# Kernel tuning notes

Hardware: AMD Instinct MI355X
Metric: run time of the kernel (lower is better)

## Reference

```python
import jax, jax.numpy as jnp
import numpy as np

B, N, IN_DIM, HID, HEADS, K = 2, 2048, 1024, 512, 8, 8
HD = HID // HEADS
EPS = 1e-5
SCALE = float(1.0 / np.sqrt(HD))

def _ln(x, g, b):
    m = jnp.mean(x, -1, keepdims=True)
    v = jnp.var(x, -1, keepdims=True)
    return (x - m) * jax.lax.rsqrt(v + EPS) * g + b

def setup_inputs() -> dict:
    key = jax.random.key(0)
    ks = jax.random.split(key, 40)
    def p(k, shape):
        return jax.random.normal(k, shape, jnp.float32) * 0.02
    z = lambda *s: jnp.zeros(s, jnp.float32)
    o = lambda *s: jnp.ones(s, jnp.float32)
    return {
        "x": jax.random.normal(ks[0], (B, N, IN_DIM), jnp.float32),
        # fc_start: Linear(in,hid) + GLU Linear(hid,2*hid)
        "w_start": p(ks[1], (HID, IN_DIM)), "b_start": z(HID),
        "glu_w": p(ks[2], (2 * HID, HID)), "glu_b": z(2 * HID),
        # 2 GCN layers (stacked on leading axis)
        "gcn_w": p(ks[3], (2, HID, HID)), "gcn_b": z(2, HID),
        "gcn_g": o(2, HID), "gcn_beta": z(2, HID),
        # 2 transformer layers
        "qkv_w": p(ks[4], (2, 3 * HID, HID)), "qkv_b": z(2, 3 * HID),
        "out_w": p(ks[5], (2, HID, HID)), "out_b": z(2, HID),
        "ln1_g": o(2, HID), "ln1_b": z(2, HID),
        "ffn_w1": p(ks[6], (2, 2 * HID, HID)), "ffn_b1": z(2, 2 * HID),
        "ffn_w2": p(ks[7], (2, HID, 2 * HID)), "ffn_b2": z(2, HID),
        "ln2_g": o(2, HID), "ln2_b": z(2, HID),
        # fusion, attention pooling, classifier
        "fus_w": p(ks[8], (HID, 2 * HID)), "fus_b": z(HID),
        "attn_w1": p(ks[9], (256, HID)), "attn_b1": z(256),
        "attn_w2": p(ks[10], (1, 256)), "attn_b2": z(1),
        "cls_w1": p(ks[11], (HID // 2, HID)), "cls_b1": z(HID // 2),
        "cls_w2": p(ks[12], (1, HID // 2)), "cls_b2": z(1),
    }

def reference(x, w_start, b_start, glu_w, glu_b, gcn_w, gcn_b, gcn_g, gcn_beta,
              qkv_w, qkv_b, out_w, out_b, ln1_g, ln1_b, ffn_w1, ffn_b1,
              ffn_w2, ffn_b2, ln2_g, ln2_b, fus_w, fus_b,
              attn_w1, attn_b1, attn_w2, attn_b2,
              cls_w1, cls_b1, cls_w2, cls_b2):
    # fc_start: Linear -> GLU (dropout off in eval)
    h = x @ w_start.T + b_start
    vg = h @ glu_w.T + glu_b
    val, gate = jnp.split(vg, 2, -1)
    h = val * jax.nn.sigmoid(gate)                      # [B,N,HID]

    # dynamic KNN graph: cdist + topk + scatter + sym-normalize
    sq = jnp.sum(h * h, -1)
    d2 = sq[:, :, None] + sq[:, None, :] - 2.0 * jnp.einsum('bnc,bmc->bnm', h, h)
    dist = jnp.sqrt(jnp.maximum(d2, 0.0))
    _, idx = jax.lax.top_k(-dist, K + 1)                # nearest K+1 (incl self)
    bi = jnp.arange(B)[:, None, None]
    ri = jnp.arange(N)[None, :, None]
    adj = jnp.zeros((B, N, N), h.dtype).at[bi, ri, idx].set(1.0)
    rs = jnp.sum(adj, -1)
    dinv = jnp.where(rs > 0, rs ** -0.5, 0.0)
    adj = adj * dinv[:, :, None] * dinv[:, None, :]     # == D^-1/2 A D^-1/2

    # GCN branch
    hg = h
    for i in range(2):
        s = hg @ gcn_w[i].T + gcn_b[i]
        o = jnp.einsum('bnm,bmc->bnc', adj, s)
        o = _ln(o, gcn_g[i], gcn_beta[i])
        hg = jax.nn.leaky_relu(o, 0.2) + hg

    # Transformer branch (post-LN)
    ht = h
    for i in range(2):
        qkv = ht @ qkv_w[i].T + qkv_b[i]
        q, k_, v = jnp.split(qkv, 3, -1)
        q = q.reshape(B, N, HEADS, HD)
        k_ = k_.reshape(B, N, HEADS, HD)
        v = v.reshape(B, N, HEADS, HD)
        att = jax.nn.softmax(jnp.einsum('bqhd,bkhd->bhqk', q, k_) * SCALE, -1)
        ao = jnp.einsum('bhqk,bkhd->bqhd', att, v).reshape(B, N, HID)
        ao = ao @ out_w[i].T + out_b[i]
        ht = _ln(ht + ao, ln1_g[i], ln1_b[i])
        ff = jax.nn.gelu(ht @ ffn_w1[i].T + ffn_b1[i], approximate=False) @ ffn_w2[i].T + ffn_b2[i]
        ht = _ln(ht + ff, ln2_g[i], ln2_b[i])

    hf = jnp.concatenate([hg, ht], -1) @ fus_w.T + fus_b  # [B,N,HID]

    # gated attention pooling
    a = jnp.tanh(hf @ attn_w1.T + attn_b1) @ attn_w2.T + attn_b2
    a = jax.nn.softmax(a, axis=1)                       # [B,N,1]
    M = jnp.sum(hf * a, axis=1)                         # [B,HID]

    logits = jax.nn.elu(M @ cls_w1.T + cls_b1) @ cls_w2.T + cls_b2  # [B,1]
    return logits, a, M
```

## Files before the change

kernel.cpp:

```cpp
#include <hip/hip_runtime.h>
#include <hip/hip_bf16.h>
#include <math.h>

#define NSEQ 2048
#define ROWS 4096
#define KNN 9
#define MB (1ull << 20)

typedef short bh8 __attribute__((ext_vector_type(8)));
typedef float f4v __attribute__((ext_vector_type(4)));
typedef unsigned long long u64k;

__device__ __forceinline__ short f2bf(float f) {
    union { float f; unsigned u; } v; v.f = f;
    unsigned r = (v.u + 0x7fffu + ((v.u >> 16) & 1u)) >> 16;
    return (short)r;
}
__device__ __forceinline__ float b2f(short s) {
    union { unsigned u; float f; } v; v.u = ((unsigned)(unsigned short)s) << 16; return v.f;
}

__device__ __forceinline__ void gload16(const void* g, void* l) {
    __builtin_amdgcn_global_load_lds(
        (const __attribute__((address_space(1))) void*)g,
        (__attribute__((address_space(3))) void*)l, 16, 0, 0);
}

__device__ __forceinline__ float blockReduceSum(float v, float* red) {
    int tid = threadIdx.x;
    red[tid] = v; __syncthreads();
    for (int s = 128; s > 0; s >>= 1) {
        if (tid < s) red[tid] += red[tid + s];
        __syncthreads();
    }
    float r = red[0]; __syncthreads();
    return r;
}

struct CvtArgs { const float* src[10]; short* dst[10]; int n4[10]; };
__global__ __launch_bounds__(256) void cvt_k(CvtArgs a) {
    int s = blockIdx.y;
    const float* sp = a.src[s]; short* dp = a.dst[s]; int n = a.n4[s];
    for (int i = blockIdx.x * 256 + threadIdx.x; i < n; i += gridDim.x * 256) {
        float4 v = ((const float4*)sp)[i];
        short4 o; o.x = f2bf(v.x); o.y = f2bf(v.y); o.z = f2bf(v.z); o.w = f2bf(v.w);
        ((short4*)dp)[i] = o;
    }
}

template <int OUTMODE>
__global__ __launch_bounds__(256) void mfma_gemm(
        const short* __restrict__ A, const short* __restrict__ W,
        const float* __restrict__ bias, float* __restrict__ Cf, short* __restrict__ Cb,
        int M, int N, int K)
{
    __shared__ short As[2][64 * 64];
    __shared__ short Bs[2][64 * 64];
    int tid = threadIdx.x;
    int wv = tid >> 6, l = tid & 63;
    int g = l >> 4, c = l & 15;
    int wr = wv >> 1, wc = wv & 1;
    int bm = blockIdx.y * 64, bn = blockIdx.x * 64;
    int sr = l >> 3, sc = ((l & 7) ^ sr) * 8;
    const short* Ap = A + (size_t)(bm + wv * 16 + sr) * K + sc;
    const short* Wp = W + (size_t)(bn + wv * 16 + sr) * K + sc;
    int ldsB = (wv * 16) * 64;

    #define GSTAGE(buf, k0) { \
        gload16(Ap + (k0), &As[buf][ldsB]); \
        gload16(Ap + (size_t)8 * K + (k0), &As[buf][ldsB + 8 * 64]); \
        gload16(Wp + (k0), &Bs[buf][ldsB]); \
        gload16(Wp + (size_t)8 * K + (k0), &Bs[buf][ldsB + 8 * 64]); }

    f4v acc[2][2] = {};
    GSTAGE(0, 0);
    __syncthreads();
    int nk = K >> 6;
    for (int t = 0; t < nk; ++t) {
        int cur = t & 1;
        if (t + 1 < nk) GSTAGE(cur ^ 1, (t + 1) << 6);
        #pragma unroll
        for (int ks = 0; ks < 2; ++ks) {
            bh8 af[2], bf_[2];
            #pragma unroll
            for (int mi = 0; mi < 2; ++mi) {
                int row = wr * 32 + mi * 16 + c;
                af[mi] = *(const bh8*)(&As[cur][row * 64 + (((ks * 4 + g) ^ (c & 7)) * 8)]);
            }
            #pragma unroll
            for (int ni = 0; ni < 2; ++ni) {
                int row = wc * 32 + ni * 16 + c;
                bf_[ni] = *(const bh8*)(&Bs[cur][row * 64 + (((ks * 4 + g) ^ (c & 7)) * 8)]);
            }
            #pragma unroll
            for (int mi = 0; mi < 2; ++mi)
                #pragma unroll
                for (int ni = 0; ni < 2; ++ni)
                    acc[mi][ni] = __builtin_amdgcn_mfma_f32_16x16x32_bf16(af[mi], bf_[ni], acc[mi][ni], 0, 0, 0);
        }
        __syncthreads();
    }
    #undef GSTAGE
    short* Kb_  = (OUTMODE == 3) ? Cb + 2097152 : nullptr;
    short* Vt_  = (OUTMODE == 3) ? Cb + 4194304 : nullptr;
    #pragma unroll
    for (int mi = 0; mi < 2; ++mi) {
        int row = bm + wr * 32 + mi * 16 + g * 4;
        #pragma unroll
        for (int ni = 0; ni < 2; ++ni) {
            int col = bn + wc * 32 + ni * 16 + c;
            float bv = bias[col];
            #pragma unroll
            for (int rr = 0; rr < 4; ++rr) {
                float v = acc[mi][ni][rr] + bv;
                if (OUTMODE == 0) Cf[(size_t)(row + rr) * N + col] = v;
                else if (OUTMODE == 1) Cb[(size_t)(row + rr) * N + col] = f2bf(v);
                else if (OUTMODE == 2) {
                    Cf[(size_t)(row + rr) * N + col] = v;
                    Cb[(size_t)(row + rr) * N + col] = f2bf(v);
                } else if (OUTMODE == 3) {
                    int b = (row + rr) >> 11, n = (row + rr) & 2047;
                    if (col < 512) {
                        int h = col >> 6, d = col & 63;
                        Cb[(((size_t)(b * 8 + h) * NSEQ + n) << 6) + d] = f2bf(v * 0.18033688f);
                    } else if (col < 1024) {
                        int cc = col - 512, h = cc >> 6, d = cc & 63;
                        Kb_[(((size_t)(b * 8 + h) * NSEQ + n) << 6) + d] = f2bf(v);
                    } else {
                        int cc = col - 1024, h = cc >> 6, d = cc & 63;
                        Vt_[(((size_t)(b * 8 + h) * NSEQ + n) << 6) + d] = f2bf(v);
                    }
                } else if (OUTMODE == 4) {
                    Cb[(size_t)(row + rr) * N + col] = f2bf(0.5f * v * (1.f + erff(v * 0.70710678118654752f)));
                } else if (OUTMODE == 5) {
                    Cf[(size_t)(row + rr) * N + col] = tanhf(v);
                }
            }
        }
    }
}

__global__ __launch_bounds__(256) void mfma_gram(
        const short* __restrict__ Hi, const short* __restrict__ Lo,
        const float* __restrict__ SQ, float* __restrict__ D2)
{
    __shared__ short HiR[64 * 64], LoR[64 * 64], HiC[64 * 64], LoC[64 * 64];
    int tid = threadIdx.x;
    int wv = tid >> 6, l = tid & 63;
    int g = l >> 4, c = l & 15;
    int wr = wv >> 1, wc = wv & 1;
    int bm = blockIdx.y * 64, bn = blockIdx.x * 64;
    int sr = l >> 3, sc = ((l & 7) ^ sr) * 8;
    const short* hiR = Hi + (size_t)(bm + wv * 16 + sr) * 512 + sc;
    const short* loR = Lo + (size_t)(bm + wv * 16 + sr) * 512 + sc;
    const short* hiC = Hi + (size_t)(bn + wv * 16 + sr) * 512 + sc;
    const short* loC = Lo + (size_t)(bn + wv * 16 + sr) * 512 + sc;
    int ldsOff = (wv * 16) * 64;
    f4v acc[2][2] = {};
    for (int k0 = 0; k0 < 512; k0 += 64) {
        __syncthreads();
        gload16(hiR + k0, HiR + ldsOff);
        gload16(hiR + (size_t)8 * 512 + k0, HiR + ldsOff + 8 * 64);
        gload16(loR + k0, LoR + ldsOff);
        gload16(loR + (size_t)8 * 512 + k0, LoR + ldsOff + 8 * 64);
        gload16(hiC + k0, HiC + ldsOff);
        gload16(hiC + (size_t)8 * 512 + k0, HiC + ldsOff + 8 * 64);
        gload16(loC + k0, LoC + ldsOff);
        gload16(loC + (size_t)8 * 512 + k0, LoC + ldsOff + 8 * 64);
        __syncthreads();
        #pragma unroll
        for (int ks = 0; ks < 2; ++ks) {
            bh8 hr[2], lr_[2], hc[2], lc[2];
            #pragma unroll
            for (int mi = 0; mi < 2; ++mi) {
                int o = (wr * 32 + mi * 16 + c) * 64 + (((ks * 4 + g) ^ (c & 7)) * 8);
                hr[mi] = *(const bh8*)(HiR + o);
                lr_[mi] = *(const bh8*)(LoR + o);
            }
            #pragma unroll
            for (int ni = 0; ni < 2; ++ni) {
                int o = (wc * 32 + ni * 16 + c) * 64 + (((ks * 4 + g) ^ (c & 7)) * 8);
                hc[ni] = *(const bh8*)(HiC + o);
                lc[ni] = *(const bh8*)(LoC + o);
            }
            #pragma unroll
            for (int mi = 0; mi < 2; ++mi)
                #pragma unroll
                for (int ni = 0; ni < 2; ++ni) {
                    acc[mi][ni] = __builtin_amdgcn_mfma_f32_16x16x32_bf16(hr[mi], hc[ni], acc[mi][ni], 0, 0, 0);
                    acc[mi][ni] = __builtin_amdgcn_mfma_f32_16x16x32_bf16(hr[mi], lc[ni], acc[mi][ni], 0, 0, 0);
                    acc[mi][ni] = __builtin_amdgcn_mfma_f32_16x16x32_bf16(lr_[mi], hc[ni], acc[mi][ni], 0, 0, 0);
                }
        }
    }
    #pragma unroll
    for (int mi = 0; mi < 2; ++mi) {
        int row = bm + wr * 32 + mi * 16 + g * 4;
        #pragma unroll
        for (int ni = 0; ni < 2; ++ni) {
            int col = bn + wc * 32 + ni * 16 + c;
            float sqc = SQ[col];
            #pragma unroll
            for (int rr = 0; rr < 4; ++rr)
                D2[(size_t)(row + rr) * NSEQ + col] = SQ[row + rr] + sqc - 2.f * acc[mi][ni][rr];
        }
    }
}

__global__ __launch_bounds__(256) void topk9_k(const float* __restrict__ D2, int* __restrict__ idx)
{
    int n = blockIdx.x, tid = threadIdx.x;
    __shared__ u64k lists[256][9];
    u64k a[8];
    union { float f; unsigned u; } cv;
    #pragma unroll
    for (int j = 0; j < 8; ++j) {
        int mcol = tid + j * 256;
        cv.f = fmaxf(D2[(size_t)n * NSEQ + mcol], 0.f);
        a[j] = ((u64k)cv.u << 32) | (unsigned)mcol;
    }
    #define CE(i,j) { u64k x = a[i], y = a[j]; bool t = x < y; a[i] = t ? x : y; a[j] = t ? y : x; }
    CE(0,1) CE(2,3) CE(4,5) CE(6,7)
    CE(0,2) CE(1,3) CE(4,6) CE(5,7)
    CE(1,2) CE(5,6)
    CE(0,4) CE(1,5) CE(2,6) CE(3,7)
    CE(2,4) CE(3,5)
    CE(1,2) CE(3,4) CE(5,6)
    #undef CE
    #pragma unroll
    for (int j = 0; j < 8; ++j) lists[tid][j] = a[j];
    lists[tid][8] = ~0ull;
    __syncthreads();
    for (int s = 128; s >= 1; s >>= 1) {
        if (tid < s) {
            u64k out[9];
            u64k* Al = lists[tid];
            u64k* Bl = lists[tid + s];
            int ia = 0, ib = 0;
            #pragma unroll
            for (int o = 0; o < 9; ++o) {
                u64k av = Al[ia], bv = Bl[ib];
                bool t = av <= bv;
                out[o] = t ? av : bv;
                ia += t; ib += !t;
            }
            #pragma unroll
            for (int o = 0; o < 9; ++o) Al[o] = out[o];
        }
        __syncthreads();
    }
    if (tid < 9) idx[n * KNN + tid] = (int)(lists[0][tid] & 0xffffffffu);
}

__global__ __launch_bounds__(256) void gcn_post(
        const float* __restrict__ s, const int* __restrict__ idx,
        const float* __restrict__ g, const float* __restrict__ be,
        float* __restrict__ hg, short* __restrict__ hgb)
{
    int row = blockIdx.x, tid = threadIdx.x;
    int bb = row >> 11;
    __shared__ float os[512];
    __shared__ float red[256];
    int id[KNN];
    #pragma unroll
    for (int j = 0; j < KNN; ++j) id[j] = idx[row * KNN + j] + (bb << 11);
    for (int c = tid; c < 512; c += 256) {
        float acc = 0.f;
        #pragma unroll
        for (int j = 0; j < KNN; ++j) acc += s[((size_t)id[j] << 9) + c];
        os[c] = acc * (1.f / 9.f);
    }
    __syncthreads();
    float mean = blockReduceSum(os[tid] + os[tid + 256], red) * (1.f / 512.f);
    float d0 = os[tid] - mean, d1 = os[tid + 256] - mean;
    float var = blockReduceSum(d0 * d0 + d1 * d1, red) * (1.f / 512.f);
    float rs = rsqrtf(var + 1e-5f);
    size_t base = (size_t)row << 9;
    for (int c = tid; c < 512; c += 256) {
        float y = (os[c] - mean) * rs * g[c] + be[c];
        y = y > 0.f ? y : 0.2f * y;
        float nv = y + hg[base + c];
        hg[base + c] = nv;
        hgb[base + c] = f2bf(nv);
    }
}

__global__ __launch_bounds__(256) void ln_res(
        float* __restrict__ x, const float* __restrict__ r,
        const float* __restrict__ g, const float* __restrict__ b, short* __restrict__ xb)
{
    int row = blockIdx.x, tid = threadIdx.x;
    __shared__ float xs[512];
    __shared__ float red[256];
    size_t base = (size_t)row << 9;
    for (int c = tid; c < 512; c += 256) xs[c] = x[base + c] + r[base + c];
    __syncthreads();
    float mean = blockReduceSum(xs[tid] + xs[tid + 256], red) * (1.f / 512.f);
    float d0 = xs[tid] - mean, d1 = xs[tid + 256] - mean;
    float var = blockReduceSum(d0 * d0 + d1 * d1, red) * (1.f / 512.f);
    float rs = rsqrtf(var + 1e-5f);
    for (int c = tid; c < 512; c += 256) {
        float y = (xs[c] - mean) * rs * g[c] + b[c];
        x[base + c] = y;
        xb[base + c] = f2bf(y);
    }
}

__global__ __launch_bounds__(256) void vtr_k(const short* __restrict__ Vtmp, short* __restrict__ Vt)
{
    int nt = blockIdx.x, bh = blockIdx.y;
    int t = threadIdx.x;
    #pragma unroll
    for (int it = 0; it < 2; ++it) {
        int idx = it * 256 + t;
        int d = idx >> 3, nc = (idx & 7) * 8;
        short tmp[8];
        #pragma unroll
        for (int j = 0; j < 8; ++j)
            tmp[j] = Vtmp[(((size_t)bh * NSEQ + nt * 64 + nc + j) << 6) + d];
        *(bh8*)(Vt + (((size_t)bh * 64 + d) << 11) + nt * 64 + nc) = *(const bh8*)tmp;
    }
}

__global__ __launch_bounds__(256) void flash_attn(
        const short* __restrict__ Qb, const short* __restrict__ Kb,
        const short* __restrict__ Vt, float* __restrict__ Op, float* __restrict__ Ml)
{
    __shared__ short Ks[2][4096];
    __shared__ short Vs[2][4096];
    __shared__ char Pl[4][2048];
    int tid = threadIdx.x;
    int wid = tid >> 6, lane = tid & 63;
    int g = lane >> 4, c = lane & 15;
    int s = blockIdx.y, bh = blockIdx.z;
    int q0 = blockIdx.x * 64 + wid * 16;
    char* myP = Pl[wid];
    int srow = lane >> 3;
    int sc8 = ((lane & 7) ^ srow) * 8;
    int w8 = wid * 8;

    const short* KbB = Kb + ((size_t)bh * NSEQ + s * (NSEQ / 2)) * 64;
    const short* VtB = Vt + (size_t)bh * 64 * NSEQ + s * (NSEQ / 2);

    const short* qbase = Qb + ((size_t)bh * NSEQ + q0 + c) * 64 + g * 8;
    bh8 qa0 = *(const bh8*)(qbase);
    bh8 qa1 = *(const bh8*)(qbase + 32);

    bh8 ones;
    #pragma unroll
    for (int j = 0; j < 8; ++j) ones[j] = (short)0x3F80;

    f4v o0 = {0,0,0,0}, o1 = {0,0,0,0}, o2 = {0,0,0,0}, o3 = {0,0,0,0};
    f4v ol = {0,0,0,0};
    float m[4] = {-INFINITY,-INFINITY,-INFINITY,-INFINITY};

    #define FSTAGE(buf, kt) { \
        const short* kp_ = KbB + (size_t)(kt) * 64 * 64; \
        gload16(kp_ + (size_t)(w8 + srow) * 64 + sc8,        &Ks[buf][w8 * 64]); \
        gload16(kp_ + (size_t)(32 + w8 + srow) * 64 + sc8,   &Ks[buf][(32 + w8) * 64]); \
        const short* vp_ = VtB + (size_t)(kt) * 64; \
        gload16(vp_ + (size_t)(w8 + srow) * NSEQ + sc8,      &Vs[buf][w8 * 64]); \
        gload16(vp_ + (size_t)(32 + w8 + srow) * NSEQ + sc8, &Vs[buf][(32 + w8) * 64]); }

    FSTAGE(0, 0);
    __syncthreads();
    for (int t = 0; t < 16; ++t) {
        int cur = t & 1;
        if (t < 15) FSTAGE(cur ^ 1, t + 1);
        f4v sv[4];
        #pragma unroll
        for (int cb = 0; cb < 4; ++cb) {
            int row = cb * 16 + c;
            const short* kr = &Ks[cur][row * 64];
            bh8 kb0 = *(const bh8*)(kr + ((g ^ (row & 7)) * 8));
            bh8 kb1 = *(const bh8*)(kr + (((4 + g) ^ (row & 7)) * 8));
            f4v a = {0,0,0,0};
            a = __builtin_amdgcn_mfma_f32_16x16x32_bf16(qa0, kb0, a, 0, 0, 0);
            a = __builtin_amdgcn_mfma_f32_16x16x32_bf16(qa1, kb1, a, 0, 0, 0);
            sv[cb] = a;
        }
        float mt[4];
        #pragma unroll
        for (int r = 0; r < 4; ++r) {
            float v = fmaxf(fmaxf(sv[0][r], sv[1][r]), fmaxf(sv[2][r], sv[3][r]));
            v = fmaxf(v, __shfl_xor(v, 1));
            v = fmaxf(v, __shfl_xor(v, 2));
            v = fmaxf(v, __shfl_xor(v, 4));
            v = fmaxf(v, __shfl_xor(v, 8));
            mt[r] = v;
        }
        bool need = (mt[0] > m[0] + 6.f) | (mt[1] > m[1] + 6.f) |
                    (mt[2] > m[2] + 6.f) | (mt[3] > m[3] + 6.f);
        if (__any(need)) {
            f4v alv;
            #pragma unroll
            for (int r = 0; r < 4; ++r) {
                float mn = fmaxf(m[r], mt[r]);
                alv[r] = __builtin_amdgcn_exp2f(m[r] - mn);
                m[r] = mn;
            }
            o0 *= alv; o1 *= alv; o2 *= alv; o3 *= alv; ol *= alv;
        }
        #pragma unroll
        for (int cb = 0; cb < 4; ++cb) {
            #pragma unroll
            for (int r = 0; r < 4; ++r) {
                float p = __builtin_amdgcn_exp2f(sv[cb][r] - m[r]);
                unsigned pk;
                asm("v_cvt_pk_bf16_f32 %0, %1, %2" : "=v"(pk) : "v"(p), "v"(p));
                int row = g * 4 + r;
                int byte = row * 128 + (((cb * 16 + c) * 2) ^ ((row & 7) << 4));
                *(short*)(myP + byte) = (short)pk;
            }
        }
        bh8 pa0 = *(const bh8*)(myP + c * 128 + (( 0 + g * 16) ^ ((c & 7) << 4)));
        bh8 pa1 = *(const bh8*)(myP + c * 128 + ((64 + g * 16) ^ ((c & 7) << 4)));
        ol = __builtin_amdgcn_mfma_f32_16x16x32_bf16(pa0, ones, ol, 0, 0, 0);
        ol = __builtin_amdgcn_mfma_f32_16x16x32_bf16(pa1, ones, ol, 0, 0, 0);
        #pragma unroll
        for (int db = 0; db < 4; ++db) {
            int row = db * 16 + c;
            const short* vr = &Vs[cur][row * 64];
            bh8 vb0 = *(const bh8*)(vr + ((g ^ (row & 7)) * 8));
            bh8 vb1 = *(const bh8*)(vr + (((4 + g) ^ (row & 7)) * 8));
            f4v* op = (db == 0) ? &o0 : (db == 1) ? &o1 : (db == 2) ? &o2 : &o3;
            *op = __builtin_amdgcn_mfma_f32_16x16x32_bf16(pa0, vb0, *op, 0, 0, 0);
            *op = __builtin_amdgcn_mfma_f32_16x16x32_bf16(pa1, vb1, *op, 0, 0, 0);
        }
        __syncthreads();
    }
    #undef FSTAGE
    #pragma unroll
    for (int r = 0; r < 4; ++r) {
        size_t rb = (((size_t)(s * 16 + bh) * NSEQ) + q0 + g * 4 + r) * 64 + c;
        Op[rb]      = o0[r];
        Op[rb + 16] = o1[r];
        Op[rb + 32] = o2[r];
        Op[rb + 48] = o3[r];
    }
    if (c == 0) {
        #pragma unroll
        for (int r = 0; r < 4; ++r) {
            size_t mb = (((size_t)(s * 16 + bh) * NSEQ) + q0 + g * 4 + r) * 2;
            Ml[mb] = m[r]; Ml[mb + 1] = ol[r];
        }
    }
}

__global__ __launch_bounds__(256) void merge_k(const float* __restrict__ Op, const float* __restrict__ Ml,
                                               short* __restrict__ aob)
{
    int idx = blockIdx.x * 256 + threadIdx.x;
    int d = idx & 63, q = (idx >> 6) & 2047, bh = idx >> 17;
    size_t r0 = (size_t)bh * NSEQ + q;
    size_t r1 = (size_t)(16 + bh) * NSEQ + q;
    float m0 = Ml[r0 * 2], l0 = Ml[r0 * 2 + 1];
    float m1 = Ml[r1 * 2], l1 = Ml[r1 * 2 + 1];
    float M = fmaxf(m0, m1);
    float w0 = __builtin_amdgcn_exp2f(m0 - M), w1 = __builtin_amdgcn_exp2f(m1 - M);
    float L = l0 * w0 + l1 * w1;
    float v = (Op[r0 * 64 + d] * w0 + Op[r1 * 64 + d] * w1) / L;
    int b = bh >> 3, h = bh & 7;
    aob[((size_t)(b * NSEQ + q)) * 512 + h * 64 + d] = f2bf(v);
}

__global__ __launch_bounds__(256) void glu_row_k(const float* __restrict__ vg, float* __restrict__ h,
        float* __restrict__ hgf, short* __restrict__ hi, short* __restrict__ lo,
        float* __restrict__ sq) {
    int row = blockIdx.x, tid = threadIdx.x;
    __shared__ float red[256];
    size_t vb = (size_t)row << 10;
    size_t hb = (size_t)row << 9;
    float ss = 0.f;
    #pragma unroll
    for (int j = 0; j < 2; ++j) {
        int c = tid + j * 256;
        float v = vg[vb + c], gt = vg[vb + 512 + c];
        float hv = v * (1.f / (1.f + __expf(-gt)));
        h[hb + c] = hv; hgf[hb + c] = hv;
        short hbb = f2bf(hv);
        hi[hb + c] = hbb;
        lo[hb + c] = f2bf(hv - b2f(hbb));
        ss = fmaf(hv, hv, ss);
    }
    float sm = blockReduceSum(ss, red);
    if (tid == 0) sq[row] = sm;
}

__global__ void concat_bf(const short* __restrict__ hgb, const short* __restrict__ htb,
                          short* __restrict__ cat) {
    for (int i = blockIdx.x * 256 + threadIdx.x; i < ROWS * 256; i += gridDim.x * 256) {
        int row = i >> 8, c4 = (i & 255) * 4;
        short4 v = (c4 < 512) ? *(const short4*)(hgb + ((size_t)row << 9) + c4)
                              : *(const short4*)(htb + ((size_t)row << 9) + c4 - 512);
        *(short4*)(cat + ((size_t)row << 10) + c4) = v;
    }
}

__global__ __launch_bounds__(256) void rowdot_k(const float* __restrict__ t, const float* __restrict__ w2,
                                                const float* __restrict__ b2, float* __restrict__ srow) {
    int row = blockIdx.x, tid = threadIdx.x;
    __shared__ float red[256];
    float s = blockReduceSum(t[(size_t)row * 256 + tid] * w2[tid], red);
    if (tid == 0) srow[row] = s + b2[0];
}
__global__ __launch_bounds__(256) void softmax_n_k(const float* __restrict__ srow, float* __restrict__ a,
                                                   float* __restrict__ out) {
    int b = blockIdx.x, tid = threadIdx.x;
    __shared__ float red[256];
    float mx = -INFINITY;
    for (int n = tid; n < NSEQ; n += 256) mx = fmaxf(mx, srow[b * NSEQ + n]);
    red[tid] = mx; __syncthreads();
    for (int s = 128; s > 0; s >>= 1) {
        if (tid < s) red[tid] = fmaxf(red[tid], red[tid + s]);
        __syncthreads();
    }
    mx = red[0]; __syncthreads();
    float sm = 0.f;
    for (int n = tid; n < NSEQ; n += 256) {
        float e = expf(srow[b * NSEQ + n] - mx);
        a[b * NSEQ + n] = e; sm += e;
    }
    float inv = 1.f / blockReduceSum(sm, red);
    for (int n = tid; n < NSEQ; n += 256) {
        float v = a[b * NSEQ + n] * inv;
        a[b * NSEQ + n] = v;
        out[2 + b * NSEQ + n] = v;
    }
}
__global__ __launch_bounds__(256) void pool_part(const float* __restrict__ hf, const float* __restrict__ a,
                                                 float* __restrict__ part) {
    int b = blockIdx.y, chunk = blockIdx.x, tid = threadIdx.x;
    float a0 = 0.f, a1 = 0.f;
    for (int r = 0; r < 64; ++r) {
        int n = chunk * 64 + r;
        float wgt = a[b * NSEQ + n];
        const float* row = hf + ((size_t)(b * NSEQ + n) << 9);
        a0 = fmaf(row[tid], wgt, a0);
        a1 = fmaf(row[tid + 256], wgt, a1);
    }
    part[((b * 32 + chunk) << 9) + tid] = a0;
    part[((b * 32 + chunk) << 9) + tid + 256] = a1;
}
__global__ __launch_bounds__(256) void pool_fin(const float* __restrict__ part, float* __restrict__ Mb,
                                                float* __restrict__ out) {
    int b = blockIdx.x, tid = threadIdx.x;
    float s0 = 0.f, s1 = 0.f;
    for (int ch = 0; ch < 32; ++ch) {
        s0 += part[((b * 32 + ch) << 9) + tid];
        s1 += part[((b * 32 + ch) << 9) + tid + 256];
    }
    Mb[b * 512 + tid] = s0; Mb[b * 512 + tid + 256] = s1;
    out[2 + ROWS + b * 512 + tid] = s0; out[2 + ROWS + b * 512 + tid + 256] = s1;
}
__global__ __launch_bounds__(256) void classifier_k(const float* __restrict__ Mb,
        const float* __restrict__ w1, const float* __restrict__ b1,
        const float* __restrict__ w2, const float* __restrict__ b2, float* __restrict__ out) {
    int b = blockIdx.x, tid = threadIdx.x;
    __shared__ float Ms[512];
    __shared__ float red[256];
    for (int c = tid; c < 512; c += 256) Ms[c] = Mb[b * 512 + c];
    __syncthreads();
    float acc = 0.f;
    for (int c = 0; c < 512; ++c) acc = fmaf(Ms[c], w1[tid * 512 + c], acc);
    acc += b1[tid];
    float hj = acc > 0.f ? acc : expm1f(acc);
    float s = blockReduceSum(hj * w2[tid], red);
    if (tid == 0) out[b] = s + b2[0];
}

extern "C" void kernel_launch(void* const* d_in, const int* in_sizes, int n_in,
                              void* d_out, int out_size, void* d_ws, size_t ws_size,
                              hipStream_t stream)
{
    const float* X      = (const float*)d_in[0];
    const float* Wstart = (const float*)d_in[1];
    const float* Bstart = (const float*)d_in[2];
    const float* GluW   = (const float*)d_in[3];
    const float* GluB   = (const float*)d_in[4];
    const float* GcnW   = (const float*)d_in[5];
    const float* GcnB   = (const float*)d_in[6];
    const float* GcnG   = (const float*)d_in[7];
    const float* GcnBe  = (const float*)d_in[8];
    const float* QkvW   = (const float*)d_in[9];
    const float* QkvB   = (const float*)d_in[10];
    const float* OutW   = (const float*)d_in[11];
    const float* OutB   = (const float*)d_in[12];
    const float* Ln1G   = (const float*)d_in[13];
    const float* Ln1B   = (const float*)d_in[14];
    const float* Ffn1W  = (const float*)d_in[15];
    const float* Ffn1B  = (const float*)d_in[16];
    const float* Ffn2W  = (const float*)d_in[17];
    const float* Ffn2B  = (const float*)d_in[18];
    const float* Ln2G   = (const float*)d_in[19];
    const float* Ln2B   = (const float*)d_in[20];
    const float* FusW   = (const float*)d_in[21];
    const float* FusB   = (const float*)d_in[22];
    const float* AW1    = (const float*)d_in[23];
    const float* AB1    = (const float*)d_in[24];
    const float* AW2    = (const float*)d_in[25];
    const float* AB2    = (const float*)d_in[26];
    const float* CW1    = (const float*)d_in[27];
    const float* CB1    = (const float*)d_in[28];
    const float* CW2    = (const float*)d_in[29];
    const float* CB2    = (const float*)d_in[30];
    float* out = (float*)d_out;

    if (ws_size < 86 * MB) return;

    char* w = (char*)d_ws;
    short* Wb = (short*)w;
    short* wbStart = Wb;
    short* wbGlu   = Wb + 524288;
    short* wbGcn   = Wb + 1048576;
    short* wbQkv   = Wb + 1572864;
    short* wbOut   = Wb + 3145728;
    short* wbFfn1  = Wb + 3670016;
    short* wbFfn2  = Wb + 4718592;
    short* wbFus   = Wb + 5767168;
    short* wbAw1   = Wb + 6291456;
    float* sq   = (float*)(w + 13 * MB);
    int*   idx  = (int*)  (w + 13 * MB + (16u << 10));
    float* srow = (float*)(w + 13 * MB + (176u << 10));
    float* afb  = (float*)(w + 13 * MB + (192u << 10));
    float* Mbuf = (float*)(w + 13 * MB + (208u << 10));
    float* part = (float*)(w + 13 * MB + (212u << 10));
    float* Ml   = (float*)(w + 13 * MB + (384u << 10));
    short* Xbf  = (short*)(w + 14 * MB);
    float* hg   = (float*)(w + 14 * MB);
    short* hpreb= (short*)(w + 22 * MB);
    short* hgb  = (short*)(w + 22 * MB);
    float* big  = (float*)(w + 26 * MB);
    float* ffn2o= (float*)(w + 42 * MB);
    float* h    = (float*)(w + 50 * MB);
    short* hhi  = (short*)(w + 58 * MB);
    short* hlo  = (short*)(w + 62 * MB);
    short* htb  = (short*)(w + 62 * MB);
    float* hf   = (float*)(w + 58 * MB);
    short* Vt   = (short*)(w + 66 * MB);
    short* hfb  = (short*)(w + 66 * MB);
    short* aob  = (short*)(w + 70 * MB);
    float* t256 = (float*)(w + 70 * MB);
    short* Qb   = (short*)(w + 74 * MB);
    short* Kb   = (short*)(w + 78 * MB);
    short* Vtmp = (short*)(w + 82 * MB);
    short* ffb  = (short*)(w + 74 * MB);
    short* catb = (short*)(w + 74 * MB);

    dim3 blk(256);

    CvtArgs ca;
    ca.src[0] = X;     ca.dst[0] = Xbf;     ca.n4[0] = ROWS * 1024 / 4;
    ca.src[1] = Wstart;ca.dst[1] = wbStart; ca.n4[1] = 524288 / 4;
    ca.src[2] = GluW;  ca.dst[2] = wbGlu;   ca.n4[2] = 524288 / 4;
    ca.src[3] = GcnW;  ca.dst[3] = wbGcn;   ca.n4[3] = 524288 / 4;
    ca.src[4] = QkvW;  ca.dst[4] = wbQkv;   ca.n4[4] = 1572864 / 4;
    ca.src[5] = OutW;  ca.dst[5] = wbOut;   ca.n4[5] = 524288 / 4;
    ca.src[6] = Ffn1W; ca.dst[6] = wbFfn1;  ca.n4[6] = 1048576 / 4;
    ca.src[7] = Ffn2W; ca.dst[7] = wbFfn2;  ca.n4[7] = 1048576 / 4;
    ca.src[8] = FusW;  ca.dst[8] = wbFus;   ca.n4[8] = 524288 / 4;
    ca.src[9] = AW1;   ca.dst[9] = wbAw1;   ca.n4[9] = 131072 / 4;
    cvt_k<<<dim3(256, 10), blk, 0, stream>>>(ca);

    mfma_gemm<1><<<dim3(8, 64), blk, 0, stream>>>(Xbf, wbStart, Bstart, nullptr, hpreb, ROWS, 512, 1024);
    mfma_gemm<0><<<dim3(16, 64), blk, 0, stream>>>(hpreb, wbGlu, GluB, big, nullptr, ROWS, 1024, 512);
    glu_row_k<<<dim3(ROWS), blk, 0, stream>>>(big, h, hg, hhi, hlo, sq);

    for (int b = 0; b < 2; ++b) {
        mfma_gram<<<dim3(32, 32), blk, 0, stream>>>(hhi + (size_t)b * NSEQ * 512,
                                                    hlo + (size_t)b * NSEQ * 512,
                                                    sq + b * NSEQ, big);
        topk9_k<<<dim3(NSEQ), blk, 0, stream>>>(big, idx + b * NSEQ * KNN);
    }

    const short* gA = hhi;
    for (int i = 0; i < 2; ++i) {
        mfma_gemm<0><<<dim3(8, 64), blk, 0, stream>>>(gA, wbGcn + (size_t)i * 262144,
                                                      GcnB + i * 512, big, nullptr, ROWS, 512, 512);
        gcn_post<<<dim3(ROWS), blk, 0, stream>>>(big, idx, GcnG + i * 512, GcnBe + i * 512, hg, hgb);
        gA = hgb;
    }

    const short* tA = hhi;
    for (int i = 0; i < 2; ++i) {
        mfma_gemm<3><<<dim3(24, 64), blk, 0, stream>>>(tA, wbQkv + (size_t)i * 786432,
                                                       QkvB + i * 1536, nullptr, Qb, ROWS, 1536, 512);
        vtr_k<<<dim3(32, 16), blk, 0, stream>>>(Vtmp, Vt);
        flash_attn<<<dim3(32, 2, 16), blk, 0, stream>>>(Qb, Kb, Vt, big, Ml);
        merge_k<<<dim3(8192), blk, 0, stream>>>(big, Ml, aob);
        mfma_gemm<0><<<dim3(8, 64), blk, 0, stream>>>(aob, wbOut + (size_t)i * 262144,
                                                      OutB + i * 512, big, nullptr, ROWS, 512, 512);
        ln_res<<<dim3(ROWS), blk, 0, stream>>>(h, big, Ln1G + i * 512, Ln1B + i * 512, htb);
        mfma_gemm<4><<<dim3(16, 64), blk, 0, stream>>>(htb, wbFfn1 + (size_t)i * 524288,
                                                       Ffn1B + i * 1024, nullptr, ffb, ROWS, 1024, 512);
        mfma_gemm<0><<<dim3(8, 64), blk, 0, stream>>>(ffb, wbFfn2 + (size_t)i * 524288,
                                                      Ffn2B + i * 512, ffn2o, nullptr, ROWS, 512, 1024);
        ln_res<<<dim3(ROWS), blk, 0, stream>>>(h, ffn2o, Ln2G + i * 512, Ln2B + i * 512, htb);
        tA = htb;
    }

    concat_bf<<<dim3(2048), blk, 0, stream>>>(hgb, htb, catb);
    mfma_gemm<2><<<dim3(8, 64), blk, 0, stream>>>(catb, wbFus, FusB, hf, hfb, ROWS, 512, 1024);

    mfma_gemm<5><<<dim3(4, 64), blk, 0, stream>>>(hfb, wbAw1, AB1, t256, nullptr, ROWS, 256, 512);
    rowdot_k<<<dim3(ROWS), blk, 0, stream>>>(t256, AW2, AB2, srow);
    softmax_n_k<<<dim3(2), blk, 0, stream>>>(srow, afb, out);
    pool_part<<<dim3(32, 2), blk, 0, stream>>>(hf, afb, part);
    pool_fin<<<dim3(2), blk, 0, stream>>>(part, Mbuf, out);

    classifier_k<<<dim3(2), blk, 0, stream>>>(Mbuf, CW1, CB1, CW2, CB2, out);
}
```

Before: 484.9 us.

## Write V transposed from QKV GEMM epilogue and keep attention probabilities in registers

The QKV GEMM epilogue now writes V directly in transposed [bh][d][n] layout with a vectorized short4 store, so the separate vtr_k transpose kernel and its launch go away. Flash attention swaps the MFMA operand order to compute S transposed, which gives one running max per lane with a single cross-lane reduction. The P tile is repacked through cross-lane shuffles instead of an LDS round trip. The row sum is accumulated in scalar registers instead of through an extra MFMA against a ones vector. The risks are shuffle overhead and correctness of the new lane mapping and output indexing.

```diff
diff --git a/kernel.cpp b/kernel.cpp
--- a/kernel.cpp
+++ b/kernel.cpp
@@ -110,30 +110,43 @@
         for (int ni = 0; ni < 2; ++ni) {
             int col = bn + wc * 32 + ni * 16 + c;
             float bv = bias[col];
-            #pragma unroll
-            for (int rr = 0; rr < 4; ++rr) {
-                float v = acc[mi][ni][rr] + bv;
-                if (OUTMODE == 0) Cf[(size_t)(row + rr) * N + col] = v;
-                else if (OUTMODE == 1) Cb[(size_t)(row + rr) * N + col] = f2bf(v);
-                else if (OUTMODE == 2) {
-                    Cf[(size_t)(row + rr) * N + col] = v;
-                    Cb[(size_t)(row + rr) * N + col] = f2bf(v);
-                } else if (OUTMODE == 3) {
-                    int b = (row + rr) >> 11, n = (row + rr) & 2047;
-                    if (col < 512) {
-                        int h = col >> 6, d = col & 63;
-                        Cb[(((size_t)(b * 8 + h) * NSEQ + n) << 6) + d] = f2bf(v * 0.18033688f);
-                    } else if (col < 1024) {
-                        int cc = col - 512, h = cc >> 6, d = cc & 63;
-                        Kb_[(((size_t)(b * 8 + h) * NSEQ + n) << 6) + d] = f2bf(v);
-                    } else {
-                        int cc = col - 1024, h = cc >> 6, d = cc & 63;
-                        Vt_[(((size_t)(b * 8 + h) * NSEQ + n) << 6) + d] = f2bf(v);
+            if (OUTMODE == 3) {
+                int b = row >> 11, n0 = row & 2047;
+                if (col < 512) {
+                    int h = col >> 6, d = col & 63;
+                    size_t base = (((size_t)(b * 8 + h) * NSEQ + n0) << 6) + d;
+                    #pragma unroll
+                    for (int rr = 0; rr < 4; ++rr)
+                        Cb[base + ((size_t)rr << 6)] = f2bf((acc[mi][ni][rr] + bv) * 0.18033688f);
+                } else if (col < 1024) {
+                    int cc = col - 512, h = cc >> 6, d = cc & 63;
+                    size_t base = (((size_t)(b * 8 + h) * NSEQ + n0) << 6) + d;
+                    #pragma unroll
+                    for (int rr = 0; rr < 4; ++rr)
+                        Kb_[base + ((size_t)rr << 6)] = f2bf(acc[mi][ni][rr] + bv);
+                } else {
+                    int cc = col - 1024, h = cc >> 6, d = cc & 63;
+                    short4 ov;
+                    ov.x = f2bf(acc[mi][ni][0] + bv);
+                    ov.y = f2bf(acc[mi][ni][1] + bv);
+                    ov.z = f2bf(acc[mi][ni][2] + bv);
+                    ov.w = f2bf(acc[mi][ni][3] + bv);
+                    *(short4*)(Vt_ + (((size_t)((b * 8 + h) * 64 + d)) << 11) + n0) = ov;
+                }
+            } else {
+                #pragma unroll
+                for (int rr = 0; rr < 4; ++rr) {
+                    float v = acc[mi][ni][rr] + bv;
+                    if (OUTMODE == 0) Cf[(size_t)(row + rr) * N + col] = v;
+                    else if (OUTMODE == 1) Cb[(size_t)(row + rr) * N + col] = f2bf(v);
+                    else if (OUTMODE == 2) {
+                        Cf[(size_t)(row + rr) * N + col] = v;
+                        Cb[(size_t)(row + rr) * N + col] = f2bf(v);
+                    } else if (OUTMODE == 4) {
+                        Cb[(size_t)(row + rr) * N + col] = f2bf(0.5f * v * (1.f + erff(v * 0.70710678118654752f)));
+                    } else if (OUTMODE == 5) {
+                        Cf[(size_t)(row + rr) * N + col] = tanhf(v);
                     }
-                } else if (OUTMODE == 4) {
-                    Cb[(size_t)(row + rr) * N + col] = f2bf(0.5f * v * (1.f + erff(v * 0.70710678118654752f)));
-                } else if (OUTMODE == 5) {
-                    Cf[(size_t)(row + rr) * N + col] = tanhf(v);
                 }
             }
         }
@@ -306,35 +319,17 @@
     }
 }
 
-__global__ __launch_bounds__(256) void vtr_k(const short* __restrict__ Vtmp, short* __restrict__ Vt)
-{
-    int nt = blockIdx.x, bh = blockIdx.y;
-    int t = threadIdx.x;
-    #pragma unroll
-    for (int it = 0; it < 2; ++it) {
-        int idx = it * 256 + t;
-        int d = idx >> 3, nc = (idx & 7) * 8;
-        short tmp[8];
-        #pragma unroll
-        for (int j = 0; j < 8; ++j)
-            tmp[j] = Vtmp[(((size_t)bh * NSEQ + nt * 64 + nc + j) << 6) + d];
-        *(bh8*)(Vt + (((size_t)bh * 64 + d) << 11) + nt * 64 + nc) = *(const bh8*)tmp;
-    }
-}
-
 __global__ __launch_bounds__(256) void flash_attn(
         const short* __restrict__ Qb, const short* __restrict__ Kb,
         const short* __restrict__ Vt, float* __restrict__ Op, float* __restrict__ Ml)
 {
     __shared__ short Ks[2][4096];
     __shared__ short Vs[2][4096];
-    __shared__ char Pl[4][2048];
     int tid = threadIdx.x;
     int wid = tid >> 6, lane = tid & 63;
     int g = lane >> 4, c = lane & 15;
     int s = blockIdx.y, bh = blockIdx.z;
     int q0 = blockIdx.x * 64 + wid * 16;
-    char* myP = Pl[wid];
     int srow = lane >> 3;
     int sc8 = ((lane & 7) ^ srow) * 8;
     int w8 = wid * 8;
@@ -346,13 +341,12 @@
     bh8 qa0 = *(const bh8*)(qbase);
     bh8 qa1 = *(const bh8*)(qbase + 32);
 
-    bh8 ones;
-    #pragma unroll
-    for (int j = 0; j < 8; ++j) ones[j] = (short)0x3F80;
-
     f4v o0 = {0,0,0,0}, o1 = {0,0,0,0}, o2 = {0,0,0,0}, o3 = {0,0,0,0};
-    f4v ol = {0,0,0,0};
-    float m[4] = {-INFINITY,-INFINITY,-INFINITY,-INFINITY};
+    float lloc = 0.f;
+    float mrun = -INFINITY;
+    int hi2 = g >> 1;
+    int s1 = c + (((g << 1) & 3) << 4);
+    int s2 = c + ((((g << 1) + 1) & 3) << 4);
 
     #define FSTAGE(buf, kt) { \
         const short* kp_ = KbB + (size_t)(kt) * 64 * 64; \
@@ -375,48 +369,54 @@
             bh8 kb0 = *(const bh8*)(kr + ((g ^ (row & 7)) * 8));
             bh8 kb1 = *(const bh8*)(kr + (((4 + g) ^ (row & 7)) * 8));
             f4v a = {0,0,0,0};
-            a = __builtin_amdgcn_mfma_f32_16x16x32_bf16(qa0, kb0, a, 0, 0, 0);
-            a = __builtin_amdgcn_mfma_f32_16x16x32_bf16(qa1, kb1, a, 0, 0, 0);
+            a = __builtin_amdgcn_mfma_f32_16x16x32_bf16(kb0, qa0, a, 0, 0, 0);
+            a = __builtin_amdgcn_mfma_f32_16x16x32_bf16(kb1, qa1, a, 0, 0, 0);
             sv[cb] = a;
         }
-        float mt[4];
-        #pragma unroll
-        for (int r = 0; r < 4; ++r) {
-            float v = fmaxf(fmaxf(sv[0][r], sv[1][r]), fmaxf(sv[2][r], sv[3][r]));
-            v = fmaxf(v, __shfl_xor(v, 1));
-            v = fmaxf(v, __shfl_xor(v, 2));
-            v = fmaxf(v, __shfl_xor(v, 4));
-            v = fmaxf(v, __shfl_xor(v, 8));
-            mt[r] = v;
-        }
-        bool need = (mt[0] > m[0] + 6.f) | (mt[1] > m[1] + 6.f) |
-                    (mt[2] > m[2] + 6.f) | (mt[3] > m[3] + 6.f);
-        if (__any(need)) {
-            f4v alv;
-            #pragma unroll
-            for (int r = 0; r < 4; ++r) {
-                float mn = fmaxf(m[r], mt[r]);
-                alv[r] = __builtin_amdgcn_exp2f(m[r] - mn);
-                m[r] = mn;
-            }
-            o0 *= alv; o1 *= alv; o2 *= alv; o3 *= alv; ol *= alv;
-        }
+        float mt = fmaxf(fmaxf(fmaxf(sv[0][0], sv[0][1]), fmaxf(sv[0][2], sv[0][3])),
+                         fmaxf(fmaxf(sv[1][0], sv[1][1]), fmaxf(sv[1][2], sv[1][3])));
+        mt = fmaxf(mt, fmaxf(fmaxf(sv[2][0], sv[2][1]), fmaxf(sv[2][2], sv[2][3])));
+        mt = fmaxf(mt, fmaxf(fmaxf(sv[3][0], sv[3][1]), fmaxf(sv[3][2], sv[3][3])));
+        mt = fmaxf(mt, __shfl_xor(mt, 16));
+        mt = fmaxf(mt, __shfl_xor(mt, 32));
+        if (__any(mt > mrun + 6.f)) {
+            float mn = fmaxf(mrun, mt);
+            float al = __builtin_amdgcn_exp2f(mrun - mn);
+            mrun = mn;
+            o0 *= al; o1 *= al; o2 *= al; o3 *= al; lloc *= al;
+        }
+        unsigned wv_[8];
         #pragma unroll
         for (int cb = 0; cb < 4; ++cb) {
-            #pragma unroll
-            for (int r = 0; r < 4; ++r) {
-                float p = __builtin_amdgcn_exp2f(sv[cb][r] - m[r]);
-                unsigned pk;
-                asm("v_cvt_pk_bf16_f32 %0, %1, %2" : "=v"(pk) : "v"(p), "v"(p));
-                int row = g * 4 + r;
-                int byte = row * 128 + (((cb * 16 + c) * 2) ^ ((row & 7) << 4));
-                *(short*)(myP + byte) = (short)pk;
-            }
-        }
-        bh8 pa0 = *(const bh8*)(myP + c * 128 + (( 0 + g * 16) ^ ((c & 7) << 4)));
-        bh8 pa1 = *(const bh8*)(myP + c * 128 + ((64 + g * 16) ^ ((c & 7) << 4)));
-        ol = __builtin_amdgcn_mfma_f32_16x16x32_bf16(pa0, ones, ol, 0, 0, 0);
-        ol = __builtin_amdgcn_mfma_f32_16x16x32_bf16(pa1, ones, ol, 0, 0, 0);
+            float p0 = __builtin_amdgcn_exp2f(sv[cb][0] - mrun);
+            float p1 = __builtin_amdgcn_exp2f(sv[cb][1] - mrun);
+            float p2 = __builtin_amdgcn_exp2f(sv[cb][2] - mrun);
+            float p3 = __builtin_amdgcn_exp2f(sv[cb][3] - mrun);
+            lloc += (p0 + p1) + (p2 + p3);
+            asm("v_cvt_pk_bf16_f32 %0, %1, %2" : "=v"(wv_[cb * 2])     : "v"(p0), "v"(p1));
+            asm("v_cvt_pk_bf16_f32 %0, %1, %2" : "=v"(wv_[cb * 2 + 1]) : "v"(p2), "v"(p3));
+        }
+        union { unsigned u[4]; bh8 h; } pa0u, pa1u;
+        {
+            unsigned t0 = __shfl((int)wv_[0], s1), t2 = __shfl((int)wv_[2], s1);
+            unsigned t1 = __shfl((int)wv_[1], s1), t3 = __shfl((int)wv_[3], s1);
+            unsigned u0 = __shfl((int)wv_[0], s2), u2 = __shfl((int)wv_[2], s2);
+            unsigned u1 = __shfl((int)wv_[1], s2), u3 = __shfl((int)wv_[3], s2);
+            pa0u.u[0] = hi2 ? t2 : t0;
+            pa0u.u[1] = hi2 ? t3 : t1;
+            pa0u.u[2] = hi2 ? u2 : u0;
+            pa0u.u[3] = hi2 ? u3 : u1;
+        }
+        {
+            unsigned t0 = __shfl((int)wv_[4], s1), t2 = __shfl((int)wv_[6], s1);
+            unsigned t1 = __shfl((int)wv_[5], s1), t3 = __shfl((int)wv_[7], s1);
+            unsigned u0 = __shfl((int)wv_[4], s2), u2 = __shfl((int)wv_[6], s2);
+            unsigned u1 = __shfl((int)wv_[5], s2), u3 = __shfl((int)wv_[7], s2);
+            pa1u.u[0] = hi2 ? t2 : t0;
+            pa1u.u[1] = hi2 ? t3 : t1;
+            pa1u.u[2] = hi2 ? u2 : u0;
+            pa1u.u[3] = hi2 ? u3 : u1;
+        }
         #pragma unroll
         for (int db = 0; db < 4; ++db) {
             int row = db * 16 + c;
@@ -424,26 +424,27 @@
             bh8 vb0 = *(const bh8*)(vr + ((g ^ (row & 7)) * 8));
             bh8 vb1 = *(const bh8*)(vr + (((4 + g) ^ (row & 7)) * 8));
             f4v* op = (db == 0) ? &o0 : (db == 1) ? &o1 : (db == 2) ? &o2 : &o3;
-            *op = __builtin_amdgcn_mfma_f32_16x16x32_bf16(pa0, vb0, *op, 0, 0, 0);
-            *op = __builtin_amdgcn_mfma_f32_16x16x32_bf16(pa1, vb1, *op, 0, 0, 0);
+            *op = __builtin_amdgcn_mfma_f32_16x16x32_bf16(vb0, pa0u.h, *op, 0, 0, 0);
+            *op = __builtin_amdgcn_mfma_f32_16x16x32_bf16(vb1, pa1u.h, *op, 0, 0, 0);
         }
         __syncthreads();
     }
     #undef FSTAGE
+    float lsum = lloc;
+    lsum += __shfl_xor(lsum, 16);
+    lsum += __shfl_xor(lsum, 32);
+    size_t qrow = ((size_t)(s * 16 + bh) * NSEQ) + q0 + c;
+    size_t rb = qrow * 64 + g * 4;
     #pragma unroll
     for (int r = 0; r < 4; ++r) {
-        size_t rb = (((size_t)(s * 16 + bh) * NSEQ) + q0 + g * 4 + r) * 64 + c;
-        Op[rb]      = o0[r];
-        Op[rb + 16] = o1[r];
-        Op[rb + 32] = o2[r];
-        Op[rb + 48] = o3[r];
-    }
-    if (c == 0) {
-        #pragma unroll
-        for (int r = 0; r < 4; ++r) {
-            size_t mb = (((size_t)(s * 16 + bh) * NSEQ) + q0 + g * 4 + r) * 2;
-            Ml[mb] = m[r]; Ml[mb + 1] = ol[r];
-        }
+        Op[rb + r]      = o0[r];
+        Op[rb + 16 + r] = o1[r];
+        Op[rb + 32 + r] = o2[r];
+        Op[rb + 48 + r] = o3[r];
+    }
+    if (g == 0) {
+        Ml[qrow * 2]     = mrun;
+        Ml[qrow * 2 + 1] = lsum;
     }
 }
 
@@ -637,13 +638,12 @@
     short* hlo  = (short*)(w + 62 * MB);
     short* htb  = (short*)(w + 62 * MB);
     float* hf   = (float*)(w + 58 * MB);
-    short* Vt   = (short*)(w + 66 * MB);
     short* hfb  = (short*)(w + 66 * MB);
     short* aob  = (short*)(w + 70 * MB);
     float* t256 = (float*)(w + 70 * MB);
     short* Qb   = (short*)(w + 74 * MB);
     short* Kb   = (short*)(w + 78 * MB);
-    short* Vtmp = (short*)(w + 82 * MB);
+    short* Vt   = (short*)(w + 82 * MB);
     short* ffb  = (short*)(w + 74 * MB);
     short* catb = (short*)(w + 74 * MB);
 
@@ -685,7 +685,6 @@
     for (int i = 0; i < 2; ++i) {
         mfma_gemm<3><<<dim3(24, 64), blk, 0, stream>>>(tA, wbQkv + (size_t)i * 786432,
                                                        QkvB + i * 1536, nullptr, Qb, ROWS, 1536, 512);
-        vtr_k<<<dim3(32, 16), blk, 0, stream>>>(Vtmp, Vt);
         flash_attn<<<dim3(32, 2, 16), blk, 0, stream>>>(Qb, Kb, Vt, big, Ml);
         merge_k<<<dim3(8192), blk, 0, stream>>>(big, Ml, aob);
         mfma_gemm<0><<<dim3(8, 64), blk, 0, stream>>>(aob, wbOut + (size_t)i * 262144,
```

After: 437.1 us. 1.11x faster.
